# Performance work log

Measured on AMD Instinct MI355X. Metric: run time of the kernel, lower is better.

The kernel has to match this reference:

```python
import jax, jax.numpy as jnp
import numpy as np

B, T, D, H = 4, 4096, 1024, 16
CAP = 0.5


def setup_inputs() -> dict:
    key = jax.random.key(0)
    ks = jax.random.split(key, 8)
    s = 0.02
    n = lambda k, shape: jax.random.normal(k, shape, dtype=jnp.float32) * s
    return {
        "x": jax.random.normal(ks[0], (B, T, D), dtype=jnp.float32),
        "w_router": n(ks[1], (D,)),
        "in_proj_w": n(ks[2], (3 * D, D)),
        "in_proj_b": jnp.zeros((3 * D,), jnp.float32),
        "out_proj_w": n(ks[3], (D, D)),
        "out_proj_b": jnp.zeros((D,), jnp.float32),
        "w1": n(ks[4], (4 * D, D)),
        "b1": jnp.zeros((4 * D,), jnp.float32),
        "w2": n(ks[5], (D, 4 * D)),
        "b2": jnp.zeros((D,), jnp.float32),
        "ln1_g": jnp.ones((D,), jnp.float32),
        "ln1_b": jnp.zeros((D,), jnp.float32),
        "ln2_g": jnp.ones((D,), jnp.float32),
        "ln2_b": jnp.zeros((D,), jnp.float32),
    }


def _ln(x, g, b, eps=1e-5):
    mu = jnp.mean(x, -1, keepdims=True)
    var = jnp.var(x, -1, keepdims=True)  # population variance, matches torch LayerNorm
    return (x - mu) * jax.lax.rsqrt(var + eps) * g + b


def reference(x, w_router, in_proj_w, in_proj_b, out_proj_w, out_proj_b,
              w1, b1, w2, b2, ln1_g, ln1_b, ln2_g, ln2_b):
    Bx, Tx, Dx = x.shape
    k = max(1, int(Tx * CAP))  # tokens routed through the block, same k for every batch row
    logits = x @ w_router  # (B,T) scalar router scores
    aux = jnp.mean(logits ** 2) * 0.01
    # top-k selection; sort indices ascending = boolean-mask gather order in torch
    idx = jnp.sort(jax.lax.top_k(logits, k)[1], axis=-1)  # (B,k)
    xs = jnp.take_along_axis(x, idx[:, :, None], axis=1)  # (B,k,D)

    h = _ln(xs, ln1_g, ln1_b)
    qkv = h @ in_proj_w.T + in_proj_b  # (B,k,3D)
    q, kk, v = jnp.split(qkv, 3, axis=-1)
    dh = Dx // H
    heads = lambda t: t.reshape(Bx, k, H, dh).transpose(0, 2, 1, 3)  # (B,H,k,dh)
    q, kk, v = heads(q), heads(kk), heads(v)
    scores = jnp.einsum('bhqd,bhkd->bhqk', q, kk) / jnp.sqrt(jnp.float32(dh))
    attn = jax.nn.softmax(scores, axis=-1)
    o = jnp.einsum('bhqk,bhkd->bhqd', attn, v).transpose(0, 2, 1, 3).reshape(Bx, k, Dx)
    o = o @ out_proj_w.T + out_proj_b
    xs = xs + o
    h2 = _ln(xs, ln2_g, ln2_b)
    ff = jax.nn.gelu(h2 @ w1.T + b1, approximate=False) @ w2.T + b2
    xs = xs + ff
    # scatter processed tokens back; unselected tokens pass through unchanged
    out = x.at[jnp.arange(Bx)[:, None], idx].set(xs)
    return out, aux
```

## Files before the change

kernel.cpp:

```cpp
#include <hip/hip_runtime.h>

#define B_    4
#define T_    4096
#define D_    1024
#define H_    16
#define DH_   64
#define KTOK  2048
#define MROWS (B_*KTOK)

typedef unsigned short u16;
typedef __attribute__((ext_vector_type(8))) short short8;
typedef __attribute__((ext_vector_type(4))) float f32x4;
typedef __attribute__((ext_vector_type(4))) unsigned int u32x4;
typedef __attribute__((ext_vector_type(2))) unsigned int u32x2;
typedef __attribute__((ext_vector_type(4))) unsigned short u16x4;

static __device__ __forceinline__ u16 f2bf(float f) {
  union { float f; unsigned int u; } a; a.f = f;
  unsigned int u = a.u;
  unsigned int r = (u + 0x7FFFu + ((u >> 16) & 1u)) >> 16;
  return (u16)r;
}

#if defined(__has_builtin)
#if __has_builtin(__builtin_amdgcn_exp2f)
#define EXP2F(x) __builtin_amdgcn_exp2f(x)
#endif
#endif
#ifndef EXP2F
#define EXP2F(x) exp2f(x)
#endif

static __device__ __forceinline__ float gelu_f(float v) {
  float x = fabsf(v) * 0.70710678118654752f;
  float t = __builtin_amdgcn_rcpf(1.0f + 0.3275911f * x);
  float p = t * (0.254829592f + t * (-0.284496736f + t * (1.421413741f +
            t * (-1.453152027f + t * 1.061405429f))));
  float e = EXP2F(-1.4426950408889634f * x * x);
  float er = 1.0f - p * e;
  er = (v < 0.0f) ? -er : er;
  return 0.5f * v * (1.0f + er);
}

static __device__ __forceinline__ unsigned int pkbf_t(float a, float b) {
  unsigned int ua = __builtin_bit_cast(unsigned int, a);
  unsigned int ub = __builtin_bit_cast(unsigned int, b);
  return __builtin_amdgcn_perm(ub, ua, 0x07060302u);
}

static __device__ __forceinline__ void gld_lds16(const u16* g, u16* l) {
  __builtin_amdgcn_global_load_lds((__attribute__((address_space(1))) void*)g,
                                   (__attribute__((address_space(3))) void*)l, 16, 0, 0);
}

#define WAITV(N) asm volatile("s_waitcnt vmcnt(" #N ")" ::: "memory")

__global__ void __launch_bounds__(256) router_kernel(const float* __restrict__ x,
    const float* __restrict__ wr, float* __restrict__ logits, float* __restrict__ auxacc)
{
  int tid = threadIdx.x; int lane = tid & 63, wave = tid >> 6;
  int row = blockIdx.x * 4 + wave;
  const float* xr = x + (size_t)row * D_;
  float dot = 0.f;
#pragma unroll
  for (int j = 0; j < 4; j++) {
    int c = j * 256 + lane * 4;
    f32x4 xv = *(const f32x4*)(xr + c);
    f32x4 wv = *(const f32x4*)(wr + c);
    dot += xv[0]*wv[0] + xv[1]*wv[1] + xv[2]*wv[2] + xv[3]*wv[3];
  }
#pragma unroll
  for (int d = 1; d < 64; d <<= 1) dot += __shfl_xor(dot, d);
  __shared__ float red[4];
  if (lane == 0) { logits[row] = dot; red[wave] = dot; }
  __syncthreads();
  if (tid == 0) {
    float a = red[0]*red[0] + red[1]*red[1] + red[2]*red[2] + red[3]*red[3];
    atomicAdd(auxacc, a);
  }
}

__global__ void __launch_bounds__(256) rank_kernel(const float* __restrict__ logits,
    int* __restrict__ rnk, int* __restrict__ idx,
    const float* __restrict__ acc, float* __restrict__ auxout)
{
  __shared__ float ll[T_];
  int b = blockIdx.y;
  int tid = threadIdx.x;
  if (b == 0 && blockIdx.x == 0 && tid == 0)
    auxout[0] = acc[0] * (0.01f / (float)(B_ * T_));
  const float* lg = logits + (size_t)b * T_;
  for (int j = tid; j < T_; j += 256) ll[j] = lg[j];
  __syncthreads();
  int t = blockIdx.x * 256 + tid;
  float my = ll[t];
  int rank = 0;
  for (int j = 0; j < T_; j += 4) {
    f32x4 lj = *(const f32x4*)&ll[j];
    rank += (lj[0] > my) || (lj[0] == my && (j+0) < t);
    rank += (lj[1] > my) || (lj[1] == my && (j+1) < t);
    rank += (lj[2] > my) || (lj[2] == my && (j+2) < t);
    rank += (lj[3] > my) || (lj[3] == my && (j+3) < t);
  }
  rnk[(size_t)b * T_ + t] = rank;
  if (rank < KTOK) idx[b * KTOK + rank] = t;
}

__global__ void __launch_bounds__(256) lnpass_kernel(const float* __restrict__ x,
    const int* __restrict__ rnk, const float* __restrict__ g, const float* __restrict__ bb,
    float* __restrict__ xs_out, u16* __restrict__ hout, float* __restrict__ out)
{
  int row = blockIdx.x;
  int tid = threadIdx.x;
  const float* srow = x + (size_t)row * D_;
  f32x4 v = *(const f32x4*)(srow + tid * 4);
  int r = rnk[row];
  if (r >= KTOK) {
    *(f32x4*)(out + (size_t)row * D_ + tid * 4) = v;
    return;
  }
  size_t mrow = (size_t)(row >> 12) * KTOK + r;
  float s  = v[0] + v[1] + v[2] + v[3];
  float sq = v[0]*v[0] + v[1]*v[1] + v[2]*v[2] + v[3]*v[3];
#pragma unroll
  for (int d = 1; d < 64; d <<= 1) { s += __shfl_xor(s, d); sq += __shfl_xor(sq, d); }
  __shared__ float rs[4], rq[4];
  int lane = tid & 63, wave = tid >> 6;
  if (lane == 0) { rs[wave] = s; rq[wave] = sq; }
  __syncthreads();
  s  = rs[0] + rs[1] + rs[2] + rs[3];
  sq = rq[0] + rq[1] + rq[2] + rq[3];
  float mean = s * (1.0f / D_);
  float var  = sq * (1.0f / D_) - mean * mean;
  float rstd = rsqrtf(var + 1e-5f);
  f32x4 gg = *(const f32x4*)(g + tid * 4);
  f32x4 bv = *(const f32x4*)(bb + tid * 4);
  *(f32x4*)(xs_out + mrow * D_ + tid * 4) = v;
  u16x4 o;
#pragma unroll
  for (int j = 0; j < 4; j++) o[j] = f2bf((v[j] - mean) * rstd * gg[j] + bv[j]);
  *(u16x4*)(hout + mrow * D_ + tid * 4) = o;
}

__global__ void __launch_bounds__(256) ln2_kernel(const float* __restrict__ src,
    const float* __restrict__ g, const float* __restrict__ bb, u16* __restrict__ hout)
{
  int row = blockIdx.x;
  int tid = threadIdx.x;
  const float* srow = src + (size_t)row * D_;
  f32x4 v = *(const f32x4*)(srow + tid * 4);
  float s  = v[0] + v[1] + v[2] + v[3];
  float sq = v[0]*v[0] + v[1]*v[1] + v[2]*v[2] + v[3]*v[3];
#pragma unroll
  for (int d = 1; d < 64; d <<= 1) { s += __shfl_xor(s, d); sq += __shfl_xor(sq, d); }
  __shared__ float rs[4], rq[4];
  int lane = tid & 63, wave = tid >> 6;
  if (lane == 0) { rs[wave] = s; rq[wave] = sq; }
  __syncthreads();
  s  = rs[0] + rs[1] + rs[2] + rs[3];
  sq = rq[0] + rq[1] + rq[2] + rq[3];
  float mean = s * (1.0f / D_);
  float var  = sq * (1.0f / D_) - mean * mean;
  float rstd = rsqrtf(var + 1e-5f);
  f32x4 gg = *(const f32x4*)(g + tid * 4);
  f32x4 bv = *(const f32x4*)(bb + tid * 4);
  u16x4 o;
#pragma unroll
  for (int j = 0; j < 4; j++) o[j] = f2bf((v[j] - mean) * rstd * gg[j] + bv[j]);
  *(u16x4*)(hout + (size_t)row * D_ + tid * 4) = o;
}

__global__ void __launch_bounds__(256) f2bf_all(const float* __restrict__ s0, const float* __restrict__ s1,
    const float* __restrict__ s2, const float* __restrict__ s3,
    u16* __restrict__ d0, u16* __restrict__ d1, u16* __restrict__ d2, u16* __restrict__ d3)
{
  const size_t c0 = (size_t)3 * D_ * D_, c1 = (size_t)4 * D_ * D_, c2 = (size_t)8 * D_ * D_;
  size_t e = (size_t)blockIdx.x * 1024 + (size_t)threadIdx.x * 4;
  const float* s; u16* d; size_t off;
  if (e < c0)      { s = s0; d = d0; off = e; }
  else if (e < c1) { s = s1; d = d1; off = e - c0; }
  else if (e < c2) { s = s2; d = d2; off = e - c1; }
  else             { s = s3; d = d3; off = e - c2; }
  f32x4 v = *(const f32x4*)(s + off);
  u16x4 o; o[0]=f2bf(v[0]); o[1]=f2bf(v[1]); o[2]=f2bf(v[2]); o[3]=f2bf(v[3]);
  *(u16x4*)(d + off) = o;
}

template<int EPI>
__global__ void __launch_bounds__(256, 2) gemm_bt(
    const u16* __restrict__ A, const u16* __restrict__ W,
    const float* __restrict__ bias, float* __restrict__ xs,
    u16* __restrict__ Cb, float* __restrict__ outf,
    const int* __restrict__ idx, u16* __restrict__ vtb, int M, int N, int K)
{
  __shared__ u16 As[2][128 * 32];
  __shared__ u16 Ws[2][128 * 32];
  const int tid = threadIdx.x;
  const int lane = tid & 63, wave = tid >> 6;
  const int wm = wave >> 1, wn = wave & 1;
  const int m16 = lane & 15, quad = lane >> 4;

  const int gx = gridDim.x;
  const int id = blockIdx.y * gx + blockIdx.x;
  const int cpx = (gx * (int)gridDim.y) >> 3;
  const int tl = (id & 7) * cpx + (id >> 3);
  const int bx = tl % gx, by = tl / gx;

  const size_t arow0 = (size_t)by * 128;
  const size_t wrow0 = (size_t)bx * 128;
  const int r4 = lane >> 2, c8 = (lane & 3) * 8;

  const u16* ag0 = A + (arow0 + wave * 16 + r4) * (size_t)K + c8;
  const u16* ag1 = ag0 + (size_t)64 * K;
  const u16* wg0 = W + (wrow0 + wave * 16 + r4) * (size_t)K + c8;
  const u16* wg1 = wg0 + (size_t)64 * K;

  auto stage = [&](int k0, int s) {
    gld_lds16(ag0 + k0, &As[s][0] + (wave * 16) * 32);
    gld_lds16(ag1 + k0, &As[s][0] + (64 + wave * 16) * 32);
    gld_lds16(wg0 + k0, &Ws[s][0] + (wave * 16) * 32);
    gld_lds16(wg1 + k0, &Ws[s][0] + (64 + wave * 16) * 32);
  };

  f32x4 acc[4][4];
#pragma unroll
  for (int i = 0; i < 4; i++)
#pragma unroll
    for (int j = 0; j < 4; j++) acc[i][j] = (f32x4)0.0f;

  stage(0, 0);
  __syncthreads();
  int cur = 0;
  for (int k0 = 0; k0 < K; k0 += 32) {
    if (k0 + 32 < K) stage(k0 + 32, cur ^ 1);
    short8 af[4], wf[4];
#pragma unroll
    for (int mt = 0; mt < 4; mt++)
      af[mt] = *(const short8*)(&As[cur][0] + (wm * 64 + mt * 16 + m16) * 32 + quad * 8);
#pragma unroll
    for (int nt = 0; nt < 4; nt++)
      wf[nt] = *(const short8*)(&Ws[cur][0] + (wn * 64 + nt * 16 + m16) * 32 + quad * 8);
#pragma unroll
    for (int mt = 0; mt < 4; mt++)
#pragma unroll
      for (int nt = 0; nt < 4; nt++)
        acc[mt][nt] = __builtin_amdgcn_mfma_f32_16x16x32_bf16(af[mt], wf[nt], acc[mt][nt], 0, 0, 0);
    __syncthreads();
    cur ^= 1;
  }

#pragma unroll
  for (int mt = 0; mt < 4; mt++) {
#pragma unroll
    for (int nt = 0; nt < 4; nt++) {
      f32x4 a = acc[mt][nt];
      size_t col = wrow0 + wn * 64 + nt * 16 + m16;
      float bvv = bias[col];
      size_t rowb = arow0 + wm * 64 + mt * 16 + quad * 4;
      if (EPI == 0) {
        if ((int)col < 2 * D_) {
          float sc = ((int)col < D_) ? 0.18033688f : 1.0f;
#pragma unroll
          for (int r = 0; r < 4; r++)
            Cb[(rowb + r) * (size_t)N + col] = f2bf((a[r] + bvv) * sc);
        } else {
          int hdh = (int)col - 2 * D_;
          int bb2 = (int)(rowb >> 11);
          int tok = (int)(rowb & (KTOK - 1));
          u16x4 o;
#pragma unroll
          for (int r = 0; r < 4; r++) o[r] = f2bf(a[r] + bvv);
          *(u16x4*)&vtb[(((size_t)(bb2 * H_) + (hdh >> 6)) * 64 + (hdh & 63)) * KTOK + tok] = o;
        }
      } else if (EPI == 1) {
#pragma unroll
        for (int r = 0; r < 4; r++) {
          size_t o = (rowb + r) * (size_t)N + col;
          xs[o] = xs[o] + (a[r] + bvv);
        }
      } else {
#pragma unroll
        for (int r = 0; r < 4; r++) {
          size_t row = rowb + r;
          int b = (int)(row >> 11);
          int i = (int)(row & (KTOK - 1));
          int t = idx[b * KTOK + i];
          float vv = xs[row * (size_t)D_ + col] + (a[r] + bvv);
          outf[((size_t)b * T_ + t) * D_ + col] = vv;
        }
      }
    }
  }
}

__global__ void __launch_bounds__(512, 1) gemm_ff1(
    const u16* __restrict__ A, const u16* __restrict__ W,
    const float* __restrict__ bias, u16* __restrict__ Cb, int M, int N, int K)
{
  __shared__ u16 Asm[2][2][128 * 64];
  __shared__ u16 Bsm[2][2][128 * 64];

  const int tid = threadIdx.x;
  const int lane = tid & 63;
  const int w = tid >> 6;
  const int m16 = lane & 15, quad = (lane >> 4) & 3;
  const int rowA = (w >> 2) * 64;
  const int rowB = (w & 3) * 32;

  const int gx = gridDim.x;
  const int id = blockIdx.y * gx + blockIdx.x;
  const int cpx = (gx * (int)gridDim.y) >> 3;
  const int tl = (id & 7) * cpx + (id >> 3);
  const int bx = tl % gx, by = tl / gx;

  const int arow0 = by * 256;
  const int wcol0 = bx * 256;

  const int th8 = tid >> 3;
  const int ccs = (tid ^ th8) & 7;
  auto stage = [&](const u16* g0, u16* l0) {
    gld_lds16(g0 + (size_t)th8 * K + ccs * 8,        l0 + (size_t)(tid & ~63) * 8);
    gld_lds16(g0 + (size_t)(64 + th8) * K + ccs * 8, l0 + 4096 + (size_t)(tid & ~63) * 8);
  };
  auto stage_tile = [&](int u, int s) {
    size_t kn = (size_t)u * 64;
    stage(A + (size_t)arow0 * K + kn,         &Asm[s][0][0]);
    stage(W + (size_t)wcol0 * K + kn,         &Bsm[s][0][0]);
    stage(A + (size_t)(arow0 + 128) * K + kn, &Asm[s][1][0]);
    stage(W + (size_t)(wcol0 + 128) * K + kn, &Bsm[s][1][0]);
  };

  auto ldA = [&](short8 (&f)[4][2], const u16* h) {
#pragma unroll
    for (int mt = 0; mt < 4; mt++) {
      int rr = rowA + mt * 16 + m16;
      int sw = rr & 7;
#pragma unroll
      for (int kk = 0; kk < 2; kk++)
        f[mt][kk] = *(const short8*)&h[rr * 64 + (((kk * 4 + quad) ^ sw) * 8)];
    }
  };
  auto ldB = [&](short8 (&f)[2][2], const u16* h) {
#pragma unroll
    for (int nt = 0; nt < 2; nt++) {
      int rb = rowB + nt * 16 + m16;
      int sw = rb & 7;
#pragma unroll
      for (int kk = 0; kk < 2; kk++)
        f[nt][kk] = *(const short8*)&h[rb * 64 + (((kk * 4 + quad) ^ sw) * 8)];
    }
  };

  f32x4 acc[4][4][2];
#pragma unroll
  for (int q = 0; q < 4; q++)
#pragma unroll
    for (int mt = 0; mt < 4; mt++)
#pragma unroll
      for (int nt = 0; nt < 2; nt++) acc[q][mt][nt] = (f32x4)0.0f;

#define MMQ(QD, FA, FB) do { \
  __builtin_amdgcn_s_setprio(1); \
  _Pragma("unroll") for (int mt = 0; mt < 4; mt++) \
  _Pragma("unroll") for (int nt = 0; nt < 2; nt++) \
  _Pragma("unroll") for (int kk = 0; kk < 2; kk++) \
    acc[QD][mt][nt] = __builtin_amdgcn_mfma_f32_16x16x32_bf16(FA[mt][kk], FB[nt][kk], acc[QD][mt][nt], 0, 0, 0); \
  __builtin_amdgcn_s_setprio(0); } while (0)

  stage_tile(0, 0);

  const int NT = K >> 6;
  short8 af[4][2], af2[4][2], bf[2][2], bf2[2][2];

  for (int t = 0; t < NT; t++) {
    const int cur = t & 1;
    const bool last = (t == NT - 1);

    WAITV(4);
    __builtin_amdgcn_s_barrier();
    __builtin_amdgcn_sched_barrier(0);
    if (!last) stage_tile(t + 1, cur ^ 1);

    ldA(af, &Asm[cur][0][0]);
    ldB(bf, &Bsm[cur][0][0]);
    MMQ(0, af, bf);

    if (last) { WAITV(0); } else { WAITV(8); }
    __builtin_amdgcn_s_barrier();
    __builtin_amdgcn_sched_barrier(0);

    ldB(bf2, &Bsm[cur][1][0]);
    MMQ(1, af, bf2);
    ldA(af2, &Asm[cur][1][0]);
    MMQ(2, af2, bf);
    MMQ(3, af2, bf2);
  }
#undef MMQ

#pragma unroll
  for (int qd = 0; qd < 4; qd++) {
    const int ha = qd >> 1, hb = qd & 1;
#pragma unroll
    for (int mt = 0; mt < 4; mt++) {
#pragma unroll
      for (int nt = 0; nt < 2; nt++) {
        f32x4 a = acc[qd][mt][nt];
        size_t col = (size_t)wcol0 + hb * 128 + (w & 3) * 32 + nt * 16 + m16;
        float bvv = bias[col];
        size_t rowb = (size_t)arow0 + ha * 128 + (w >> 2) * 64 + mt * 16 + quad * 4;
#pragma unroll
        for (int r = 0; r < 4; r++)
          Cb[(rowb + r) * (size_t)N + col] = f2bf(gelu_f(a[r] + bvv));
      }
    }
  }
}

#define PSTR 72
__global__ void __launch_bounds__(256, 3) attn_kernel(const u16* __restrict__ qkv,
                                                      const u16* __restrict__ vtb,
                                                      u16* __restrict__ obuf)
{
  __shared__ u16 Ks[2][64 * 64];
  __shared__ u16 Vs[2][64 * 64];
  __shared__ u16 Ps[4][16 * PSTR];

  const int tid = threadIdx.x;
  const int lane = tid & 63, wave = tid >> 6;
  const int m16 = lane & 15, quad = lane >> 4;
  const int bh = blockIdx.x;
  const int b = bh >> 4, h = bh & 15;
  const int q0 = blockIdx.y * 128 + wave * 32;

  const u16* base = qkv + ((size_t)b * KTOK) * (3 * D_) + h * DH_;
  const u16* vb   = vtb + (size_t)bh * 64 * KTOK;

  short8 qf[2][2];
#pragma unroll
  for (int qh = 0; qh < 2; qh++) {
    const u16* qrow = base + (size_t)(q0 + qh * 16 + m16) * (3 * D_);
    qf[qh][0] = *(const short8*)(qrow + quad * 8);
    qf[qh][1] = *(const short8*)(qrow + 32 + quad * 8);
  }

  f32x4 oacc[2][4];
#pragma unroll
  for (int qh = 0; qh < 2; qh++)
#pragma unroll
    for (int nt = 0; nt < 4; nt++) oacc[qh][nt] = (f32x4)0.0f;
  f32x4 lsum[2] = {(f32x4)0.0f, (f32x4)0.0f};

  auto stage_tile = [&](const u16* g0, size_t rstride, u16* lds) {
#pragma unroll
    for (int c = 0; c < 2; c++) {
      int g = c * 256 + tid;
      int key = g >> 3;
      int cc = (g ^ key) & 7;
      gld_lds16(g0 + (size_t)key * rstride + cc * 8,
                lds + (size_t)(c * 256 + (tid & ~63)) * 8);
    }
  };

  stage_tile(base + D_, 3 * D_, &Ks[0][0]);
  stage_tile(vb, KTOK, &Vs[0][0]);
  __syncthreads();

  int buf = 0;
  for (int tk = 0; tk < KTOK; tk += 64) {
    if (tk + 64 < KTOK) {
      stage_tile(base + (size_t)(tk + 64) * (3 * D_) + D_, 3 * D_, &Ks[buf ^ 1][0]);
      stage_tile(vb + (tk + 64), KTOK, &Vs[buf ^ 1][0]);
    }
    const u16* Kb = &Ks[buf][0];
    const u16* Vb = &Vs[buf][0];

    f32x4 sacc[2][4];
#pragma unroll
    for (int qh = 0; qh < 2; qh++)
#pragma unroll
      for (int nt = 0; nt < 4; nt++) sacc[qh][nt] = (f32x4)0.0f;
    __builtin_amdgcn_s_setprio(1);
#pragma unroll
    for (int nt = 0; nt < 4; nt++) {
      int row = nt * 16 + m16;
      int sw = row & 7;
      short8 kf0 = *(const short8*)&Kb[row * 64 + ((quad ^ sw) * 8)];
      short8 kf1 = *(const short8*)&Kb[row * 64 + (((4 + quad) ^ sw) * 8)];
#pragma unroll
      for (int qh = 0; qh < 2; qh++) {
        sacc[qh][nt] = __builtin_amdgcn_mfma_f32_16x16x32_bf16(kf0, qf[qh][0], sacc[qh][nt], 0, 0, 0);
        sacc[qh][nt] = __builtin_amdgcn_mfma_f32_16x16x32_bf16(kf1, qf[qh][1], sacc[qh][nt], 0, 0, 0);
      }
    }
    __builtin_amdgcn_s_setprio(0);

    short8 vf[4][2];
#pragma unroll
    for (int nt = 0; nt < 4; nt++) {
      int row = nt * 16 + m16;
      int sw = row & 7;
      vf[nt][0] = *(const short8*)&Vb[row * 64 + ((quad ^ sw) * 8)];
      vf[nt][1] = *(const short8*)&Vb[row * 64 + (((4 + quad) ^ sw) * 8)];
    }

#pragma unroll
    for (int qh = 0; qh < 2; qh++) {
#pragma unroll
      for (int nt = 0; nt < 4; nt++) {
        f32x4 p;
#pragma unroll
        for (int r = 0; r < 4; r++) p[r] = EXP2F(sacc[qh][nt][r]);
        lsum[qh] += p;
        u32x2 w2; w2[0] = pkbf_t(p[0], p[1]); w2[1] = pkbf_t(p[2], p[3]);
        *(u32x2*)&Ps[wave][m16 * PSTR + nt * 16 + quad * 4] = w2;
      }
      short8 pa0 = *(const short8*)&Ps[wave][m16 * PSTR + quad * 8];
      short8 pa1 = *(const short8*)&Ps[wave][m16 * PSTR + 32 + quad * 8];
      __builtin_amdgcn_s_setprio(1);
#pragma unroll
      for (int nt = 0; nt < 4; nt++) {
        oacc[qh][nt] = __builtin_amdgcn_mfma_f32_16x16x32_bf16(pa0, vf[nt][0], oacc[qh][nt], 0, 0, 0);
        oacc[qh][nt] = __builtin_amdgcn_mfma_f32_16x16x32_bf16(pa1, vf[nt][1], oacc[qh][nt], 0, 0, 0);
      }
      __builtin_amdgcn_s_setprio(0);
    }

    __syncthreads();
    buf ^= 1;
  }

  float rl[2][4];
#pragma unroll
  for (int qh = 0; qh < 2; qh++) {
    float l = (lsum[qh][0] + lsum[qh][1]) + (lsum[qh][2] + lsum[qh][3]);
    l += __shfl_xor(l, 16);
    l += __shfl_xor(l, 32);
#pragma unroll
    for (int r = 0; r < 4; r++) {
      float lr = __shfl(l, (lane & 48) | (quad * 4 + r));
      rl[qh][r] = 1.0f / lr;
    }
  }

#pragma unroll
  for (int qh = 0; qh < 2; qh++)
#pragma unroll
    for (int nt = 0; nt < 4; nt++)
#pragma unroll
      for (int r = 0; r < 4; r++) {
        int qq = q0 + qh * 16 + quad * 4 + r;
        float v = oacc[qh][nt][r] * rl[qh][r];
        obuf[((size_t)b * KTOK + qq) * D_ + h * DH_ + nt * 16 + m16] = f2bf(v);
      }
}

extern "C" void kernel_launch(void* const* d_in, const int* in_sizes, int n_in,
                              void* d_out, int out_size, void* d_ws, size_t ws_size,
                              hipStream_t stream)
{
  (void)in_sizes; (void)n_in; (void)out_size; (void)ws_size;
  const float* x          = (const float*)d_in[0];
  const float* w_router   = (const float*)d_in[1];
  const float* in_proj_w  = (const float*)d_in[2];
  const float* in_proj_b  = (const float*)d_in[3];
  const float* out_proj_w = (const float*)d_in[4];
  const float* out_proj_b = (const float*)d_in[5];
  const float* w1         = (const float*)d_in[6];
  const float* b1         = (const float*)d_in[7];
  const float* w2         = (const float*)d_in[8];
  const float* b2         = (const float*)d_in[9];
  const float* ln1g       = (const float*)d_in[10];
  const float* ln1b       = (const float*)d_in[11];
  const float* ln2g       = (const float*)d_in[12];
  const float* ln2b       = (const float*)d_in[13];
  float* out = (float*)d_out;

  char* w = (char*)d_ws;
  auto alloc = [&](size_t bytes) -> char* {
    char* p = w; w += (bytes + 255) & ~(size_t)255; return p;
  };
  float* logits = (float*)alloc((size_t)B_ * T_ * 4);
  int*   rnk    = (int*)  alloc((size_t)B_ * T_ * 4);
  int*   idx    = (int*)  alloc((size_t)B_ * KTOK * 4);
  float* auxacc = (float*)alloc(256);
  u16* inpw  = (u16*)alloc((size_t)3 * D_ * D_ * 2);
  u16* outpw = (u16*)alloc((size_t)D_ * D_ * 2);
  u16* w1b   = (u16*)alloc((size_t)4 * D_ * D_ * 2);
  u16* w2b   = (u16*)alloc((size_t)4 * D_ * D_ * 2);
  float* xs  = (float*)alloc((size_t)MROWS * D_ * 4);
  u16* hbuf  = (u16*)alloc((size_t)MROWS * D_ * 2);
  char* region = alloc((size_t)MROWS * 4 * D_ * 2);
  u16* qkvb = (u16*)region;
  u16* obuf = (u16*)(region + (size_t)MROWS * 3 * D_ * 2);
  u16* ffb  = (u16*)region;
  u16* vtb  = (u16*)alloc((size_t)B_ * H_ * DH_ * KTOK * 2);

  (void)hipMemsetAsync(auxacc, 0, 4, stream);

  router_kernel<<<B_ * T_ / 4, 256, 0, stream>>>(x, w_router, logits, auxacc);
  rank_kernel<<<dim3(T_ / 256, B_), 256, 0, stream>>>(logits, rnk, idx, auxacc,
                                                      out + (size_t)B_ * T_ * D_);
  lnpass_kernel<<<B_ * T_, 256, 0, stream>>>(x, rnk, ln1g, ln1b, xs, hbuf, out);

  f2bf_all<<<12 * D_ * D_ / 1024, 256, 0, stream>>>(in_proj_w, out_proj_w, w1, w2,
                                                    inpw, outpw, w1b, w2b);

  gemm_bt<0><<<dim3(3 * D_ / 128, MROWS / 128), 256, 0, stream>>>(
      hbuf, inpw, in_proj_b, nullptr, qkvb, nullptr, nullptr, vtb, MROWS, 3 * D_, D_);
  attn_kernel<<<dim3(B_ * H_, KTOK / 128), 256, 0, stream>>>(qkvb, vtb, obuf);
  gemm_bt<1><<<dim3(D_ / 128, MROWS / 128), 256, 0, stream>>>(
      obuf, outpw, out_proj_b, xs, nullptr, nullptr, nullptr, nullptr, MROWS, D_, D_);
  ln2_kernel<<<MROWS, 256, 0, stream>>>(xs, ln2g, ln2b, hbuf);
  gemm_ff1<<<dim3(4 * D_ / 256, MROWS / 256), 512, 0, stream>>>(
      hbuf, w1b, b1, ffb, MROWS, 4 * D_, D_);
  gemm_bt<3><<<dim3(D_ / 128, MROWS / 128), 256, 0, stream>>>(
      ffb, w2b, b2, xs, nullptr, out, idx, nullptr, MROWS, D_, 4 * D_);
}
```

Baseline: 739.0 us.

## Rework gemm_bt to BK=64 swizzled LDS tiles with split-phase waits

New measurement: 713.5 us. 1.04x faster.

```diff
diff --git a/kernel.cpp b/kernel.cpp
--- a/kernel.cpp
+++ b/kernel.cpp
@@ -193,12 +193,11 @@
     u16* __restrict__ Cb, float* __restrict__ outf,
     const int* __restrict__ idx, u16* __restrict__ vtb, int M, int N, int K)
 {
-  __shared__ u16 As[2][128 * 32];
-  __shared__ u16 Ws[2][128 * 32];
+  __shared__ u16 As[2][128 * 64];
+  __shared__ u16 Ws[2][128 * 64];
   const int tid = threadIdx.x;
   const int lane = tid & 63, wave = tid >> 6;
-  const int wm = wave >> 1, wn = wave & 1;
-  const int m16 = lane & 15, quad = lane >> 4;
+  const int m16 = lane & 15, quad = (lane >> 4) & 3;
 
   const int gx = gridDim.x;
   const int id = blockIdx.y * gx + blockIdx.x;
@@ -208,85 +207,131 @@
 
   const size_t arow0 = (size_t)by * 128;
   const size_t wrow0 = (size_t)bx * 128;
-  const int r4 = lane >> 2, c8 = (lane & 3) * 8;
-
-  const u16* ag0 = A + (arow0 + wave * 16 + r4) * (size_t)K + c8;
-  const u16* ag1 = ag0 + (size_t)64 * K;
-  const u16* wg0 = W + (wrow0 + wave * 16 + r4) * (size_t)K + c8;
-  const u16* wg1 = wg0 + (size_t)64 * K;
-
-  auto stage = [&](int k0, int s) {
-    gld_lds16(ag0 + k0, &As[s][0] + (wave * 16) * 32);
-    gld_lds16(ag1 + k0, &As[s][0] + (64 + wave * 16) * 32);
-    gld_lds16(wg0 + k0, &Ws[s][0] + (wave * 16) * 32);
-    gld_lds16(wg1 + k0, &Ws[s][0] + (64 + wave * 16) * 32);
-  };
-
-  f32x4 acc[4][4];
-#pragma unroll
-  for (int i = 0; i < 4; i++)
-#pragma unroll
-    for (int j = 0; j < 4; j++) acc[i][j] = (f32x4)0.0f;
-
-  stage(0, 0);
-  __syncthreads();
-  int cur = 0;
-  for (int k0 = 0; k0 < K; k0 += 32) {
-    if (k0 + 32 < K) stage(k0 + 32, cur ^ 1);
-    short8 af[4], wf[4];
-#pragma unroll
-    for (int mt = 0; mt < 4; mt++)
-      af[mt] = *(const short8*)(&As[cur][0] + (wm * 64 + mt * 16 + m16) * 32 + quad * 8);
-#pragma unroll
-    for (int nt = 0; nt < 4; nt++)
-      wf[nt] = *(const short8*)(&Ws[cur][0] + (wn * 64 + nt * 16 + m16) * 32 + quad * 8);
-#pragma unroll
-    for (int mt = 0; mt < 4; mt++)
+
+  const int trow = tid >> 3;
+  const int tcc  = (tid ^ trow) & 7;
+  auto stagepc = [&](const u16* g0, u16* l0) {
+    gld_lds16(g0 + (size_t)trow * K + tcc * 8,        l0 + (size_t)(tid & ~63) * 8);
+    gld_lds16(g0 + (size_t)(32 + trow) * K + tcc * 8, l0 + 2048 + (size_t)(tid & ~63) * 8);
+  };
+  auto stage_tile = [&](int u, int s) {
+    size_t kn = (size_t)u * 64;
+    stagepc(A + (arow0)      * K + kn, &As[s][0]);
+    stagepc(A + (arow0 + 64) * K + kn, &As[s][64 * 64]);
+    stagepc(W + (wrow0)      * K + kn, &Ws[s][0]);
+    stagepc(W + (wrow0 + 64) * K + kn, &Ws[s][64 * 64]);
+  };
+
+  auto ldA = [&](short8 (&f)[2][2], const u16* h) {
+#pragma unroll
+    for (int mt = 0; mt < 2; mt++) {
+      int rr = wave * 32 + mt * 16 + m16;
+      int sw = rr & 7;
+#pragma unroll
+      for (int kk = 0; kk < 2; kk++)
+        f[mt][kk] = *(const short8*)&h[rr * 64 + (((kk * 4 + quad) ^ sw) * 8)];
+    }
+  };
+  auto ldB = [&](short8 (&f)[4][2], const u16* h, int half) {
+#pragma unroll
+    for (int nt = 0; nt < 4; nt++) {
+      int rb = half * 64 + nt * 16 + m16;
+      int sw = rb & 7;
+#pragma unroll
+      for (int kk = 0; kk < 2; kk++)
+        f[nt][kk] = *(const short8*)&h[rb * 64 + (((kk * 4 + quad) ^ sw) * 8)];
+    }
+  };
+
+  f32x4 acc[2][8];
+#pragma unroll
+  for (int mt = 0; mt < 2; mt++)
+#pragma unroll
+    for (int n = 0; n < 8; n++) acc[mt][n] = (f32x4)0.0f;
+
+  stage_tile(0, 0);
+
+  const int NT = K >> 6;
+  short8 af[2][2], bf[4][2], bf2[4][2];
+
+  for (int t = 0; t < NT; t++) {
+    const int cur = t & 1;
+    const bool last = (t == NT - 1);
+
+    WAITV(2);
+    __builtin_amdgcn_s_barrier();
+    __builtin_amdgcn_sched_barrier(0);
+    if (!last) stage_tile(t + 1, cur ^ 1);
+
+    ldA(af, &As[cur][0]);
+    ldB(bf, &Ws[cur][0], 0);
+    __builtin_amdgcn_s_setprio(1);
+#pragma unroll
+    for (int mt = 0; mt < 2; mt++)
 #pragma unroll
       for (int nt = 0; nt < 4; nt++)
-        acc[mt][nt] = __builtin_amdgcn_mfma_f32_16x16x32_bf16(af[mt], wf[nt], acc[mt][nt], 0, 0, 0);
-    __syncthreads();
-    cur ^= 1;
-  }
-
-#pragma unroll
-  for (int mt = 0; mt < 4; mt++) {
-#pragma unroll
-    for (int nt = 0; nt < 4; nt++) {
-      f32x4 a = acc[mt][nt];
-      size_t col = wrow0 + wn * 64 + nt * 16 + m16;
-      float bvv = bias[col];
-      size_t rowb = arow0 + wm * 64 + mt * 16 + quad * 4;
-      if (EPI == 0) {
-        if ((int)col < 2 * D_) {
-          float sc = ((int)col < D_) ? 0.18033688f : 1.0f;
-#pragma unroll
-          for (int r = 0; r < 4; r++)
-            Cb[(rowb + r) * (size_t)N + col] = f2bf((a[r] + bvv) * sc);
+#pragma unroll
+        for (int kk = 0; kk < 2; kk++)
+          acc[mt][nt] = __builtin_amdgcn_mfma_f32_16x16x32_bf16(af[mt][kk], bf[nt][kk], acc[mt][nt], 0, 0, 0);
+    __builtin_amdgcn_s_setprio(0);
+
+    if (last) { WAITV(0); } else { WAITV(8); }
+    __builtin_amdgcn_s_barrier();
+    __builtin_amdgcn_sched_barrier(0);
+
+    ldB(bf2, &Ws[cur][0], 1);
+    __builtin_amdgcn_s_setprio(1);
+#pragma unroll
+    for (int mt = 0; mt < 2; mt++)
+#pragma unroll
+      for (int nt = 0; nt < 4; nt++)
+#pragma unroll
+        for (int kk = 0; kk < 2; kk++)
+          acc[mt][4 + nt] = __builtin_amdgcn_mfma_f32_16x16x32_bf16(af[mt][kk], bf2[nt][kk], acc[mt][4 + nt], 0, 0, 0);
+    __builtin_amdgcn_s_setprio(0);
+  }
+
+#pragma unroll
+  for (int half = 0; half < 2; half++) {
+#pragma unroll
+    for (int mt = 0; mt < 2; mt++) {
+#pragma unroll
+      for (int nt = 0; nt < 4; nt++) {
+        f32x4 a = acc[mt][half * 4 + nt];
+        size_t col = wrow0 + half * 64 + nt * 16 + m16;
+        float bvv = bias[col];
+        size_t rowb = arow0 + wave * 32 + mt * 16 + quad * 4;
+        if (EPI == 0) {
+          if ((int)col < 2 * D_) {
+            float sc = ((int)col < D_) ? 0.18033688f : 1.0f;
+#pragma unroll
+            for (int r = 0; r < 4; r++)
+              Cb[(rowb + r) * (size_t)N + col] = f2bf((a[r] + bvv) * sc);
+          } else {
+            int hdh = (int)col - 2 * D_;
+            int bb2 = (int)(rowb >> 11);
+            int tok = (int)(rowb & (KTOK - 1));
+            u16x4 o;
+#pragma unroll
+            for (int r = 0; r < 4; r++) o[r] = f2bf(a[r] + bvv);
+            *(u16x4*)&vtb[(((size_t)(bb2 * H_) + (hdh >> 6)) * 64 + (hdh & 63)) * KTOK + tok] = o;
+          }
+        } else if (EPI == 1) {
+#pragma unroll
+          for (int r = 0; r < 4; r++) {
+            size_t o = (rowb + r) * (size_t)N + col;
+            xs[o] = xs[o] + (a[r] + bvv);
+          }
         } else {
-          int hdh = (int)col - 2 * D_;
-          int bb2 = (int)(rowb >> 11);
-          int tok = (int)(rowb & (KTOK - 1));
-          u16x4 o;
-#pragma unroll
-          for (int r = 0; r < 4; r++) o[r] = f2bf(a[r] + bvv);
-          *(u16x4*)&vtb[(((size_t)(bb2 * H_) + (hdh >> 6)) * 64 + (hdh & 63)) * KTOK + tok] = o;
-        }
-      } else if (EPI == 1) {
-#pragma unroll
-        for (int r = 0; r < 4; r++) {
-          size_t o = (rowb + r) * (size_t)N + col;
-          xs[o] = xs[o] + (a[r] + bvv);
-        }
-      } else {
-#pragma unroll
-        for (int r = 0; r < 4; r++) {
-          size_t row = rowb + r;
-          int b = (int)(row >> 11);
-          int i = (int)(row & (KTOK - 1));
-          int t = idx[b * KTOK + i];
-          float vv = xs[row * (size_t)D_ + col] + (a[r] + bvv);
-          outf[((size_t)b * T_ + t) * D_ + col] = vv;
+#pragma unroll
+          for (int r = 0; r < 4; r++) {
+            size_t row = rowb + r;
+            int b = (int)(row >> 11);
+            int i = (int)(row & (KTOK - 1));
+            int t = idx[b * KTOK + i];
+            float vv = xs[row * (size_t)D_ + col] + (a[r] + bvv);
+            outf[((size_t)b * T_ + t) * D_ + col] = vv;
+          }
         }
       }
     }
@@ -423,7 +468,7 @@
 {
   __shared__ u16 Ks[2][64 * 64];
   __shared__ u16 Vs[2][64 * 64];
-  __shared__ u16 Ps[4][16 * PSTR];
+  __shared__ u16 Ps[4][2][16 * PSTR];
 
   const int tid = threadIdx.x;
   const int lane = tid & 63, wave = tid >> 6;
@@ -512,18 +557,24 @@
         for (int r = 0; r < 4; r++) p[r] = EXP2F(sacc[qh][nt][r]);
         lsum[qh] += p;
         u32x2 w2; w2[0] = pkbf_t(p[0], p[1]); w2[1] = pkbf_t(p[2], p[3]);
-        *(u32x2*)&Ps[wave][m16 * PSTR + nt * 16 + quad * 4] = w2;
+        *(u32x2*)&Ps[wave][qh][m16 * PSTR + nt * 16 + quad * 4] = w2;
       }
-      short8 pa0 = *(const short8*)&Ps[wave][m16 * PSTR + quad * 8];
-      short8 pa1 = *(const short8*)&Ps[wave][m16 * PSTR + 32 + quad * 8];
-      __builtin_amdgcn_s_setprio(1);
+    }
+    short8 pa[2][2];
+#pragma unroll
+    for (int qh = 0; qh < 2; qh++) {
+      pa[qh][0] = *(const short8*)&Ps[wave][qh][m16 * PSTR + quad * 8];
+      pa[qh][1] = *(const short8*)&Ps[wave][qh][m16 * PSTR + 32 + quad * 8];
+    }
+    __builtin_amdgcn_s_setprio(1);
+#pragma unroll
+    for (int qh = 0; qh < 2; qh++)
 #pragma unroll
       for (int nt = 0; nt < 4; nt++) {
-        oacc[qh][nt] = __builtin_amdgcn_mfma_f32_16x16x32_bf16(pa0, vf[nt][0], oacc[qh][nt], 0, 0, 0);
-        oacc[qh][nt] = __builtin_amdgcn_mfma_f32_16x16x32_bf16(pa1, vf[nt][1], oacc[qh][nt], 0, 0, 0);
+        oacc[qh][nt] = __builtin_amdgcn_mfma_f32_16x16x32_bf16(pa[qh][0], vf[nt][0], oacc[qh][nt], 0, 0, 0);
+        oacc[qh][nt] = __builtin_amdgcn_mfma_f32_16x16x32_bf16(pa[qh][1], vf[nt][1], oacc[qh][nt], 0, 0, 0);
       }
-      __builtin_amdgcn_s_setprio(0);
-    }
+    __builtin_amdgcn_s_setprio(0);
 
     __syncthreads();
     buf ^= 1;
```
